# Kernel tuning notes

Hardware: AMD Instinct MI355X
Metric: run time of the kernel (lower is better)

## Reference

```python
import jax, jax.numpy as jnp
import numpy as np

N_NODES = 30000
N_EDGES = 480000
N_REL = 16
DIM = 128
N_TRIPLES = 200000


def _xavier(key, shape):
    fan_in, fan_out = shape[-2], shape[-1]
    limit = np.sqrt(6.0 / (fan_in + fan_out)).astype(np.float32)
    return jax.random.uniform(key, shape, jnp.float32, -limit, limit)


def setup_inputs() -> dict:
    key = jax.random.key(0)
    ks = jax.random.split(key, 12)
    inp = {
        "node_emb": _xavier(ks[0], (N_NODES, DIM)),
        "rel_emb": _xavier(ks[1], (N_REL, DIM)),
        "W_rel0": _xavier(ks[2], (N_REL, DIM, DIM)),
        "Wself_w0": _xavier(ks[3], (DIM, DIM)),
        "Wself_b0": jnp.zeros((DIM,), jnp.float32),
        "W_rel1": _xavier(ks[4], (N_REL, DIM, DIM)),
        "Wself_w1": _xavier(ks[5], (DIM, DIM)),
        "Wself_b1": jnp.zeros((DIM,), jnp.float32),
        "local_nodes": jnp.arange(N_NODES, dtype=jnp.int32),
        "edge_index": jax.random.randint(ks[6], (2, N_EDGES), 0, N_NODES, jnp.int32),
        "edge_type": jax.random.randint(ks[7], (N_EDGES,), 0, N_REL, jnp.int32),
        "h_loc": jax.random.randint(ks[8], (N_TRIPLES,), 0, N_NODES, jnp.int32),
        "r_ids": jax.random.randint(ks[9], (N_TRIPLES,), 0, N_REL, jnp.int32),
        "t_loc": jax.random.randint(ks[10], (N_TRIPLES,), 0, N_NODES, jnp.int32),
    }
    return inp


def _rgcn_layer(x, edge_index, edge_type, W_rel, Ww, Wb):
    # x: [N, in], W_rel: [R, in, out], Ww: [out, in] (torch Linear layout)
    N = x.shape[0]
    out = x @ Ww.T + Wb                                 # self loop [N, out]
    src, dst = edge_index[0], edge_index[1]
    # transform every node under every relation, then gather per edge:
    # math-equivalent to bmm(x[src][:,None,:], W_rel[rel]) in the original,
    # but avoids materializing [E, in, out].
    xt = jnp.einsum('ni,rio->rno', x, W_rel)            # [R, N, out]
    msg = xt[edge_type, src]                            # [E, out]
    agg = jax.ops.segment_sum(msg, dst, num_segments=N)  # [N, out]
    deg = jax.ops.segment_sum(jnp.ones(dst.shape, x.dtype), dst, num_segments=N)
    deg = jnp.maximum(deg, 1.0)[:, None]
    return jax.nn.relu(out + agg / deg)


def reference(node_emb, rel_emb, W_rel0, Wself_w0, Wself_b0,
              W_rel1, Wself_w1, Wself_b1,
              local_nodes, edge_index, edge_type, h_loc, r_ids, t_loc):
    x = node_emb[local_nodes]                           # [N, d]
    x = _rgcn_layer(x, edge_index, edge_type, W_rel0, Wself_w0, Wself_b0)
    x = _rgcn_layer(x, edge_index, edge_type, W_rel1, Wself_w1, Wself_b1)
    # DistMult scoring on local embeddings
    scores = jnp.sum(x[h_loc] * rel_emb[r_ids] * x[t_loc], axis=-1)  # [B]
    return scores
```

## Files before the change

kernel.cpp:

```cpp
#include <hip/hip_runtime.h>

#define NN 30000
#define NE 480000
#define NR 16
#define D  128
#define NT 200000
#define BR 64
#define NBLK 469
#define NBINS (NBLK * NR)
#define GS 92
#define PF 23


__global__ void k_gather_x(const float* __restrict__ node_emb,
                           const int* __restrict__ local_nodes,
                           float* __restrict__ x) {
  int i4 = blockIdx.x * blockDim.x + threadIdx.x;
  if (i4 >= NN * (D / 4)) return;
  int n = i4 >> 5, c = i4 & 31;
  int src = local_nodes[n];
  reinterpret_cast<float4*>(x)[i4] =
      reinterpret_cast<const float4*>(node_emb)[(size_t)src * 32 + c];
}

__global__ void k_hist_bins(const int* __restrict__ ei, const int* __restrict__ et,
                            int* __restrict__ bins) {
  int e = blockIdx.x * blockDim.x + threadIdx.x;
  if (e >= NE) return;
  int d = ei[NE + e], r = et[e];
  atomicAdd(&bins[(d >> 6) * NR + r], 1);
}

__global__ void k_scan_bins(const int* __restrict__ bins, int* __restrict__ off,
                            int* __restrict__ cur) {
  __shared__ int ps[1024];
  const int t = threadIdx.x;
  const int base = t * 8;
  int c[8], s0 = 0;
#pragma unroll
  for (int u = 0; u < 8; ++u) {
    int b = base + u;
    c[u] = (b < NBINS) ? bins[b] : 0;
    s0 += c[u];
  }
  ps[t] = s0;
  __syncthreads();
  for (int dstep = 1; dstep < 1024; dstep <<= 1) {
    int v = (t >= dstep) ? ps[t - dstep] : 0;
    __syncthreads();
    ps[t] += v;
    __syncthreads();
  }
  int ex = ps[t] - s0;
#pragma unroll
  for (int u = 0; u < 8; ++u) {
    int b = base + u;
    if (b <= NBINS) {
      off[b] = ex;
      if (b < NBINS) cur[b] = ex;
    }
    ex += c[u];
  }
}

__global__ void k_fill(const int* __restrict__ ei, const int* __restrict__ et,
                       int* __restrict__ cur, int* __restrict__ srt,
                       float* __restrict__ deg) {
  int e = blockIdx.x * blockDim.x + threadIdx.x;
  if (e >= NE) return;
  int s = ei[e], d = ei[NE + e], r = et[e];
  int p = atomicAdd(&cur[(d >> 6) * NR + r], 1);
  srt[p] = ((d & 63) << 16) | s;
  atomicAdd(&deg[d], 1.0f);
}

__global__ void k_transposeW(const float* __restrict__ W0, const float* __restrict__ W1,
                             float* __restrict__ T0, float* __restrict__ T1) {
  const float* W = blockIdx.x ? W1 : W0;
  float* T = blockIdx.x ? T1 : T0;
  for (int idx = threadIdx.x; idx < D * D; idx += 256) {
    int o = idx >> 7, k = idx & 127;
    T[k * D + o] = W[idx];
  }
}

__device__ __forceinline__ void gl_lds4(const float* g, float* l) {
  __builtin_amdgcn_global_load_lds(
      (const __attribute__((address_space(1))) void*)g,
      (__attribute__((address_space(3))) void*)l, 4, 0, 0);
}


__device__ __forceinline__ void gemm_tile(const float (*S)[D],
                                          const float* __restrict__ Wg,
                                          int tx, int ty, float acc[8][4]) {
  const float4* __restrict__ W4 = reinterpret_cast<const float4*>(Wg);
#pragma unroll 8
  for (int k = 0; k < D; k += 4) {
    float4 a[8];
#pragma unroll
    for (int j = 0; j < 8; ++j)
      a[j] = *reinterpret_cast<const float4*>(&S[ty + 8 * j][k]);
    float4 w[4];
#pragma unroll
    for (int kk = 0; kk < 4; ++kk) w[kk] = W4[(k + kk) * 32 + tx];
#pragma unroll
    for (int kk = 0; kk < 4; ++kk) {
#pragma unroll
      for (int j = 0; j < 8; ++j) {
        float av = (kk == 0) ? a[j].x : (kk == 1) ? a[j].y
                 : (kk == 2) ? a[j].z : a[j].w;
        acc[j][0] += av * w[kk].x;
        acc[j][1] += av * w[kk].y;
        acc[j][2] += av * w[kk].z;
        acc[j][3] += av * w[kk].w;
      }
    }
  }
}

__launch_bounds__(256, 2)
__global__ void k_fused(const float* __restrict__ x, const float* __restrict__ Wrel,
                        const float* __restrict__ WT, const float* __restrict__ Wb,
                        const int* __restrict__ srt, const int* __restrict__ off,
                        const float* __restrict__ deg, float* __restrict__ xo) {
  __shared__ float S[BR][D];
  __shared__ float G[GS][D];
  __shared__ int dls[GS];
  const int nb = blockIdx.x;
  const int row0 = nb * BR;
  const int tx = threadIdx.x & 31, ty = threadIdx.x >> 5;
  const int wave = threadIdx.x >> 6, lane = threadIdx.x & 63;
  const float2* __restrict__ x2 = reinterpret_cast<const float2*>(x);

  float acc[8][4];
#pragma unroll
  for (int j = 0; j < 8; ++j)
#pragma unroll
    for (int m = 0; m < 4; ++m) acc[j][m] = 0.f;

  auto zeroS = [&]() {
    float4* S4 = reinterpret_cast<float4*>(&S[0][0]);
#pragma unroll
    for (int t = 0; t < 8; ++t)
      S4[threadIdx.x + 256 * t] = make_float4(0.f, 0.f, 0.f, 0.f);
  };

  auto issueDMA = [&](int b) {
    const int base = off[b], end = off[b + 1];
#pragma unroll
    for (int t = 0; t < PF; ++t) {
      int s = wave + 4 * t;
      int i = base + s;
      int p = (i < end) ? srt[i] : -1;
      if (lane == 0) dls[s] = p;
      if (p >= 0) {
        const float* row = x + (size_t)(p & 0xFFFF) * D;
        gl_lds4(row + lane, &G[s][0]);
        gl_lds4(row + 64 + lane, &G[s][64]);
      }
    }
  };
  auto depositE = [&](int b) {
#pragma unroll
    for (int t = 0; t < PF; ++t) {
      int s = wave + 4 * t;
      int p = dls[s];
      if (p >= 0) {
        float2 v = *reinterpret_cast<const float2*>(&G[s][2 * lane]);
        atomicAdd(&S[p >> 16][2 * lane], v.x);
        atomicAdd(&S[p >> 16][2 * lane + 1], v.y);
      }
    }
    const int end = off[b + 1];
    for (int i = off[b] + GS + wave; i < end; i += 4) {
      int p = srt[i];
      float2 vv = x2[(size_t)(p & 0xFFFF) * 64 + lane];
      atomicAdd(&S[p >> 16][2 * lane], vv.x);
      atomicAdd(&S[p >> 16][2 * lane + 1], vv.y);
    }
  };

  zeroS();
  issueDMA(nb * NR);
  __syncthreads();

  for (int r = 0; r < NR; ++r) {
    depositE(nb * NR + r);
    __syncthreads();
    if (r + 1 < NR) issueDMA(nb * NR + r + 1);
    gemm_tile(S, Wrel + (size_t)r * D * D, tx, ty, acc);
    __syncthreads();
    if (r + 1 < NR) {
      zeroS();
      __syncthreads();
    }
  }

#pragma unroll
  for (int j = 0; j < 8; ++j) {
    int row = row0 + ty + 8 * j;
    float dv = (row < NN) ? deg[row] : 1.f;
    float inv = 1.f / fmaxf(dv, 1.f);
#pragma unroll
    for (int m = 0; m < 4; ++m) acc[j][m] *= inv;
  }

#pragma unroll
  for (int t = 0; t < 8; ++t) {
    int idx = threadIdx.x + 256 * t;
    int rw = idx >> 5, c = idx & 31;
    float4 vv = make_float4(0.f, 0.f, 0.f, 0.f);
    if (row0 + rw < NN)
      vv = reinterpret_cast<const float4*>(x)[(size_t)(row0 + rw) * 32 + c];
    *reinterpret_cast<float4*>(&S[rw][4 * c]) = vv;
  }
  __syncthreads();
  gemm_tile(S, WT, tx, ty, acc);

  const float4 bb = reinterpret_cast<const float4*>(Wb)[tx];
#pragma unroll
  for (int j = 0; j < 8; ++j) {
    int row = row0 + ty + 8 * j;
    if (row < NN) {
      float4 o;
      o.x = fmaxf(acc[j][0] + bb.x, 0.f);
      o.y = fmaxf(acc[j][1] + bb.y, 0.f);
      o.z = fmaxf(acc[j][2] + bb.z, 0.f);
      o.w = fmaxf(acc[j][3] + bb.w, 0.f);
      reinterpret_cast<float4*>(xo + (size_t)row * D)[tx] = o;
    }
  }
}


__global__ void k_score(const float* __restrict__ x, const float* __restrict__ rel,
                        const int* __restrict__ hh, const int* __restrict__ rr,
                        const int* __restrict__ tt, float* __restrict__ out) {
  int gw = (blockIdx.x * blockDim.x + threadIdx.x) >> 6;
  int lane = threadIdx.x & 63;
  int nw = (gridDim.x * blockDim.x) >> 6;
  for (int i = gw; i < NT; i += nw) {
    const float2* ph = reinterpret_cast<const float2*>(x + (size_t)hh[i] * D);
    const float2* pr = reinterpret_cast<const float2*>(rel + (size_t)rr[i] * D);
    const float2* pt = reinterpret_cast<const float2*>(x + (size_t)tt[i] * D);
    float2 a = ph[lane], b = pr[lane], c = pt[lane];
    float v = a.x * b.x * c.x + a.y * b.y * c.y;
#pragma unroll
    for (int m = 32; m; m >>= 1) v += __shfl_xor(v, m);
    if (lane == 0) out[i] = v;
  }
}


extern "C" void kernel_launch(void* const* d_in, const int* in_sizes, int n_in,
                              void* d_out, int out_size, void* d_ws, size_t ws_size,
                              hipStream_t stream) {
  const float* node_emb = (const float*)d_in[0];
  const float* rel_emb  = (const float*)d_in[1];
  const float* W_rel0   = (const float*)d_in[2];
  const float* Wself_w0 = (const float*)d_in[3];
  const float* Wself_b0 = (const float*)d_in[4];
  const float* W_rel1   = (const float*)d_in[5];
  const float* Wself_w1 = (const float*)d_in[6];
  const float* Wself_b1 = (const float*)d_in[7];
  const int* local_nodes = (const int*)d_in[8];
  const int* edge_index  = (const int*)d_in[9];
  const int* edge_type   = (const int*)d_in[10];
  const int* h_loc = (const int*)d_in[11];
  const int* r_ids = (const int*)d_in[12];
  const int* t_loc = (const int*)d_in[13];
  float* out = (float*)d_out;

  char* ws = (char*)d_ws;
  float* x_a = (float*)(ws + 0);
  float* x_b = (float*)(ws + 15360000);
  float* WT0 = (float*)(ws + 30720000);
  float* WT1 = (float*)(ws + 30785536);
  float* deg = (float*)(ws + 30851072);
  int* bins  = (int*)(ws + 30971072);
  int* off   = (int*)(ws + 31001088);
  int* cur   = (int*)(ws + 31031108);
  int* srt   = (int*)(ws + 31061124);
  if (ws_size < (size_t)32981124) return;

  hipMemsetAsync(ws + 30851072, 0, 150016, stream);

  k_gather_x<<<3750, 256, 0, stream>>>(node_emb, local_nodes, x_a);
  k_hist_bins<<<1875, 256, 0, stream>>>(edge_index, edge_type, bins);
  k_scan_bins<<<1, 1024, 0, stream>>>(bins, off, cur);
  k_fill<<<1875, 256, 0, stream>>>(edge_index, edge_type, cur, srt, deg);
  k_transposeW<<<2, 256, 0, stream>>>(Wself_w0, Wself_w1, WT0, WT1);

  k_fused<<<NBLK, 256, 0, stream>>>(x_a, W_rel0, WT0, Wself_b0, srt, off, deg, x_b);
  k_fused<<<NBLK, 256, 0, stream>>>(x_b, W_rel1, WT1, Wself_b1, srt, off, deg, x_a);

  k_score<<<1024, 256, 0, stream>>>(x_a, rel_emb, h_loc, r_ids, t_loc, out);
}
```

Baseline: 1.449 ms.

## Replace FP32 scalar GEMM tiles with split-bf16 MFMA and swizzled LDS layout

Replaces the per-relation FP32 FMA GEMM in the fused RGCN layer with MFMA 16x16x32 bf16 instructions. Each operand is split into high and low bf16 parts (three products) to stay close to FP32 accuracy. A new pre-pack kernel converts relation and self-loop weights into MFMA fragment order. The LDS aggregation tile gets an XOR swizzle to avoid bank conflicts on the new access pattern. The cost is three MFMAs per tile, per-iteration conversion work, and slightly lower precision than exact FP32.

```diff
diff --git a/kernel.cpp b/kernel.cpp
--- a/kernel.cpp
+++ b/kernel.cpp
@@ -11,6 +11,17 @@
 #define GS 92
 #define PF 23
 
+typedef short bf16x8 __attribute__((ext_vector_type(8)));
+typedef float f32x4 __attribute__((ext_vector_type(4)));
+
+__device__ __forceinline__ unsigned short f2bf(float f) {
+  unsigned u = __float_as_uint(f);
+  return (unsigned short)((u + 0x7FFF + ((u >> 16) & 1)) >> 16);
+}
+__device__ __forceinline__ float bf2f(unsigned short h) {
+  return __uint_as_float(((unsigned)h) << 16);
+}
+
 
 __global__ void k_gather_x(const float* __restrict__ node_emb,
                            const int* __restrict__ local_nodes,
@@ -74,13 +85,20 @@
   atomicAdd(&deg[d], 1.0f);
 }
 
-__global__ void k_transposeW(const float* __restrict__ W0, const float* __restrict__ W1,
-                             float* __restrict__ T0, float* __restrict__ T1) {
-  const float* W = blockIdx.x ? W1 : W0;
-  float* T = blockIdx.x ? T1 : T0;
-  for (int idx = threadIdx.x; idx < D * D; idx += 256) {
-    int o = idx >> 7, k = idx & 127;
-    T[k * D + o] = W[idx];
+__global__ void k_packW(const float* __restrict__ Wr, const float* __restrict__ Ws,
+                        unsigned short* __restrict__ out) {
+  const int r = blockIdx.x;
+  for (int i = threadIdx.x; i < 16384; i += 256) {
+    int e = i & 7, l = (i >> 3) & 63, nt = (i >> 9) & 7, kt = i >> 12;
+    int k = kt * 32 + ((e >> 2) << 4) + (((l >> 4) & 3) << 2) + (e & 3);
+    int n = nt * 16 + (l & 15);
+    float w = (r < 16) ? Wr[((size_t)r << 14) + (k << 7) + n]
+                       : Ws[(n << 7) + k];
+    unsigned short h = f2bf(w);
+    unsigned short lo = f2bf(w - bf2f(h));
+    size_t base = ((((size_t)r * 4 + kt) * 8 + nt) * 2) * 512 + (size_t)l * 8 + e;
+    out[base] = h;
+    out[base + 512] = lo;
   }
 }
 
@@ -91,37 +109,39 @@
 }
 
 
-__device__ __forceinline__ void gemm_tile(const float (*S)[D],
-                                          const float* __restrict__ Wg,
-                                          int tx, int ty, float acc[8][4]) {
-  const float4* __restrict__ W4 = reinterpret_cast<const float4*>(Wg);
-#pragma unroll 8
-  for (int k = 0; k < D; k += 4) {
-    float4 a[8];
-#pragma unroll
-    for (int j = 0; j < 8; ++j)
-      a[j] = *reinterpret_cast<const float4*>(&S[ty + 8 * j][k]);
-    float4 w[4];
-#pragma unroll
-    for (int kk = 0; kk < 4; ++kk) w[kk] = W4[(k + kk) * 32 + tx];
-#pragma unroll
-    for (int kk = 0; kk < 4; ++kk) {
-#pragma unroll
-      for (int j = 0; j < 8; ++j) {
-        float av = (kk == 0) ? a[j].x : (kk == 1) ? a[j].y
-                 : (kk == 2) ? a[j].z : a[j].w;
-        acc[j][0] += av * w[kk].x;
-        acc[j][1] += av * w[kk].y;
-        acc[j][2] += av * w[kk].z;
-        acc[j][3] += av * w[kk].w;
-      }
-    }
-  }
-}
+#define CVT1(e, val) { unsigned short h_ = f2bf(val); ah[e] = (short)h_; \
+                       al[e] = (short)f2bf((val) - bf2f(h_)); }
+
+__device__ __forceinline__ void mfma_rel(const float (*S)[D],
+                                         const bf16x8* __restrict__ Wf,
+                                         int lane, int wave, f32x4 acc[8]) {
+  const int m = lane & 15, kg = lane >> 4;
+  const int row = wave * 16 + m;
+  const int sw = (row & 7) << 2;
+#pragma unroll
+  for (int kt = 0; kt < 4; ++kt) {
+    float4 v0 = *reinterpret_cast<const float4*>(&S[row][((kt * 8 + kg) ^ sw) << 2]);
+    float4 v1 = *reinterpret_cast<const float4*>(&S[row][((kt * 8 + 4 + kg) ^ sw) << 2]);
+    bf16x8 ah, al;
+    CVT1(0, v0.x) CVT1(1, v0.y) CVT1(2, v0.z) CVT1(3, v0.w)
+    CVT1(4, v1.x) CVT1(5, v1.y) CVT1(6, v1.z) CVT1(7, v1.w)
+    const bf16x8* Wk = Wf + (size_t)kt * 1024 + lane;
+#pragma unroll
+    for (int nt = 0; nt < 8; ++nt) {
+      bf16x8 bh = Wk[nt * 128];
+      bf16x8 bl = Wk[nt * 128 + 64];
+      acc[nt] = __builtin_amdgcn_mfma_f32_16x16x32_bf16(ah, bh, acc[nt], 0, 0, 0);
+      acc[nt] = __builtin_amdgcn_mfma_f32_16x16x32_bf16(al, bh, acc[nt], 0, 0, 0);
+      acc[nt] = __builtin_amdgcn_mfma_f32_16x16x32_bf16(ah, bl, acc[nt], 0, 0, 0);
+    }
+  }
+}
+
 
 __launch_bounds__(256, 2)
-__global__ void k_fused(const float* __restrict__ x, const float* __restrict__ Wrel,
-                        const float* __restrict__ WT, const float* __restrict__ Wb,
+__global__ void k_fused(const float* __restrict__ x,
+                        const unsigned short* __restrict__ Wpk,
+                        const float* __restrict__ Wb,
                         const int* __restrict__ srt, const int* __restrict__ off,
                         const float* __restrict__ deg, float* __restrict__ xo) {
   __shared__ float S[BR][D];
@@ -129,15 +149,13 @@
   __shared__ int dls[GS];
   const int nb = blockIdx.x;
   const int row0 = nb * BR;
-  const int tx = threadIdx.x & 31, ty = threadIdx.x >> 5;
   const int wave = threadIdx.x >> 6, lane = threadIdx.x & 63;
   const float2* __restrict__ x2 = reinterpret_cast<const float2*>(x);
-
-  float acc[8][4];
-#pragma unroll
-  for (int j = 0; j < 8; ++j)
-#pragma unroll
-    for (int m = 0; m < 4; ++m) acc[j][m] = 0.f;
+  const bf16x8* __restrict__ Wf = reinterpret_cast<const bf16x8*>(Wpk);
+
+  f32x4 acc[8];
+#pragma unroll
+  for (int nt = 0; nt < 8; ++nt) acc[nt] = 0.f;
 
   auto zeroS = [&]() {
     float4* S4 = reinterpret_cast<float4*>(&S[0][0]);
@@ -145,7 +163,6 @@
     for (int t = 0; t < 8; ++t)
       S4[threadIdx.x + 256 * t] = make_float4(0.f, 0.f, 0.f, 0.f);
   };
-
   auto issueDMA = [&](int b) {
     const int base = off[b], end = off[b + 1];
 #pragma unroll
@@ -168,16 +185,20 @@
       int p = dls[s];
       if (p >= 0) {
         float2 v = *reinterpret_cast<const float2*>(&G[s][2 * lane]);
-        atomicAdd(&S[p >> 16][2 * lane], v.x);
-        atomicAdd(&S[p >> 16][2 * lane + 1], v.y);
+        int dl = p >> 16;
+        float* dst = &S[dl][(((lane >> 1) ^ ((dl & 7) << 2)) << 2) + ((lane & 1) << 1)];
+        atomicAdd(dst, v.x);
+        atomicAdd(dst + 1, v.y);
       }
     }
     const int end = off[b + 1];
     for (int i = off[b] + GS + wave; i < end; i += 4) {
       int p = srt[i];
       float2 vv = x2[(size_t)(p & 0xFFFF) * 64 + lane];
-      atomicAdd(&S[p >> 16][2 * lane], vv.x);
-      atomicAdd(&S[p >> 16][2 * lane + 1], vv.y);
+      int dl = p >> 16;
+      float* dst = &S[dl][(((lane >> 1) ^ ((dl & 7) << 2)) << 2) + ((lane & 1) << 1)];
+      atomicAdd(dst, vv.x);
+      atomicAdd(dst + 1, vv.y);
     }
   };
 
@@ -189,7 +210,7 @@
     depositE(nb * NR + r);
     __syncthreads();
     if (r + 1 < NR) issueDMA(nb * NR + r + 1);
-    gemm_tile(S, Wrel + (size_t)r * D * D, tx, ty, acc);
+    mfma_rel(S, Wf + (size_t)r * 4096, lane, wave, acc);
     __syncthreads();
     if (r + 1 < NR) {
       zeroS();
@@ -197,13 +218,14 @@
     }
   }
 
-#pragma unroll
-  for (int j = 0; j < 8; ++j) {
-    int row = row0 + ty + 8 * j;
+  const int kg = lane >> 4;
+#pragma unroll
+  for (int j = 0; j < 4; ++j) {
+    int row = row0 + wave * 16 + kg * 4 + j;
     float dv = (row < NN) ? deg[row] : 1.f;
     float inv = 1.f / fmaxf(dv, 1.f);
 #pragma unroll
-    for (int m = 0; m < 4; ++m) acc[j][m] *= inv;
+    for (int nt = 0; nt < 8; ++nt) acc[nt][j] *= inv;
   }
 
 #pragma unroll
@@ -213,22 +235,20 @@
     float4 vv = make_float4(0.f, 0.f, 0.f, 0.f);
     if (row0 + rw < NN)
       vv = reinterpret_cast<const float4*>(x)[(size_t)(row0 + rw) * 32 + c];
-    *reinterpret_cast<float4*>(&S[rw][4 * c]) = vv;
+    *reinterpret_cast<float4*>(&S[rw][(c ^ ((rw & 7) << 2)) << 2]) = vv;
   }
   __syncthreads();
-  gemm_tile(S, WT, tx, ty, acc);
-
-  const float4 bb = reinterpret_cast<const float4*>(Wb)[tx];
-#pragma unroll
-  for (int j = 0; j < 8; ++j) {
-    int row = row0 + ty + 8 * j;
-    if (row < NN) {
-      float4 o;
-      o.x = fmaxf(acc[j][0] + bb.x, 0.f);
-      o.y = fmaxf(acc[j][1] + bb.y, 0.f);
-      o.z = fmaxf(acc[j][2] + bb.z, 0.f);
-      o.w = fmaxf(acc[j][3] + bb.w, 0.f);
-      reinterpret_cast<float4*>(xo + (size_t)row * D)[tx] = o;
+  mfma_rel(S, Wf + (size_t)16 * 4096, lane, wave, acc);
+
+#pragma unroll
+  for (int nt = 0; nt < 8; ++nt) {
+    int col = nt * 16 + (lane & 15);
+    float b = Wb[col];
+#pragma unroll
+    for (int j = 0; j < 4; ++j) {
+      int row = row0 + wave * 16 + kg * 4 + j;
+      if (row < NN)
+        xo[(size_t)row * D + col] = fmaxf(acc[nt][j] + b, 0.f);
     }
   }
 }
@@ -275,25 +295,26 @@
   char* ws = (char*)d_ws;
   float* x_a = (float*)(ws + 0);
   float* x_b = (float*)(ws + 15360000);
-  float* WT0 = (float*)(ws + 30720000);
-  float* WT1 = (float*)(ws + 30785536);
-  float* deg = (float*)(ws + 30851072);
-  int* bins  = (int*)(ws + 30971072);
-  int* off   = (int*)(ws + 31001088);
-  int* cur   = (int*)(ws + 31031108);
-  int* srt   = (int*)(ws + 31061124);
-  if (ws_size < (size_t)32981124) return;
-
-  hipMemsetAsync(ws + 30851072, 0, 150016, stream);
+  float* deg = (float*)(ws + 30720000);
+  int* bins  = (int*)(ws + 30840000);
+  int* off   = (int*)(ws + 30870016);
+  int* cur   = (int*)(ws + 30900036);
+  int* srt   = (int*)(ws + 30930052);
+  unsigned short* Wpk0 = (unsigned short*)(ws + 32850064);
+  unsigned short* Wpk1 = (unsigned short*)(ws + 33964176);
+  if (ws_size < (size_t)35078288) return;
+
+  hipMemsetAsync(ws + 30720000, 0, 150016, stream);
 
   k_gather_x<<<3750, 256, 0, stream>>>(node_emb, local_nodes, x_a);
   k_hist_bins<<<1875, 256, 0, stream>>>(edge_index, edge_type, bins);
   k_scan_bins<<<1, 1024, 0, stream>>>(bins, off, cur);
   k_fill<<<1875, 256, 0, stream>>>(edge_index, edge_type, cur, srt, deg);
-  k_transposeW<<<2, 256, 0, stream>>>(Wself_w0, Wself_w1, WT0, WT1);
-
-  k_fused<<<NBLK, 256, 0, stream>>>(x_a, W_rel0, WT0, Wself_b0, srt, off, deg, x_b);
-  k_fused<<<NBLK, 256, 0, stream>>>(x_b, W_rel1, WT1, Wself_b1, srt, off, deg, x_a);
+  k_packW<<<17, 256, 0, stream>>>(W_rel0, Wself_w0, Wpk0);
+  k_packW<<<17, 256, 0, stream>>>(W_rel1, Wself_w1, Wpk1);
+
+  k_fused<<<NBLK, 256, 0, stream>>>(x_a, Wpk0, Wself_b0, srt, off, deg, x_b);
+  k_fused<<<NBLK, 256, 0, stream>>>(x_b, Wpk1, Wself_b1, srt, off, deg, x_a);
 
   k_score<<<1024, 256, 0, stream>>>(x_a, rel_emb, h_loc, r_ids, t_loc, out);
 }
```

New measurement: 1.346 ms. 1.08x faster.
